# Performance work log

Measured on AMD Instinct MI355X. Metric: run time of the kernel, lower is better.

Reference implementation:

```python
import jax, jax.numpy as jnp
import numpy as np

EPS = 1e-12  # F.normalize eps


def setup_inputs() -> dict:
    key = jax.random.key(0)
    ks = jax.random.split(key, 12)
    N_NODES, N_EDGES, VOCAB, D = 100000, 1600000, 200000, 128
    return {
        "ent_embs": jax.random.normal(ks[0], (VOCAB, D), dtype=jnp.float32),
        "rel_embs": jax.random.normal(ks[1], (500, D), dtype=jnp.float32),
        "e_r_bias": jax.random.normal(ks[2], (N_NODES, D), dtype=jnp.float32),
        "out_norm": jax.random.uniform(ks[3], (N_NODES, 1), dtype=jnp.float32),
        "weight_neighbor": jax.random.normal(ks[4], (D, D), dtype=jnp.float32) * 0.05,
        "gru_w_ih": jax.random.normal(ks[5], (3 * D, 2 * D), dtype=jnp.float32) * 0.05,
        "gru_w_hh": jax.random.normal(ks[6], (3 * D, D), dtype=jnp.float32) * 0.05,
        "gru_b_ih": jnp.zeros((3 * D,), dtype=jnp.float32),
        "gru_b_hh": jnp.zeros((3 * D,), dtype=jnp.float32),
        "node_id": jax.random.randint(ks[7], (N_NODES,), 0, VOCAB, dtype=jnp.int64) if jax.config.jax_enable_x64 else jax.random.randint(ks[7], (N_NODES,), 0, VOCAB).astype(jnp.int32),
        "edge_src": jax.random.randint(ks[8], (N_EDGES,), 0, N_NODES).astype(jnp.int32),
        "edge_dst": jax.random.randint(ks[9], (N_EDGES,), 0, N_NODES).astype(jnp.int32),
        "g_idx": 0,
    }


def gru_cell(x, h, w_ih, w_hh, b_ih, b_hh):
    # torch.nn.GRUCell semantics; gates stacked as [r, z, n]
    gx = x @ w_ih.T + b_ih            # [N, 3D]
    gh = h @ w_hh.T + b_hh            # [N, 3D]
    xr, xz, xn = jnp.split(gx, 3, axis=1)
    hr, hz, hn = jnp.split(gh, 3, axis=1)
    r = jax.nn.sigmoid(xr + hr)
    z = jax.nn.sigmoid(xz + hz)
    n = jnp.tanh(xn + r * hn)
    return (1.0 - z) * n + z * h


def reference(ent_embs, rel_embs, e_r_bias, out_norm, weight_neighbor,
              gru_w_ih, gru_w_hh, gru_b_ih, gru_b_hh,
              node_id, edge_src, edge_dst, g_idx):
    n_nodes = e_r_bias.shape[0]
    # gather node embeddings, transform once per node (equivalent to per-edge mm)
    h = ent_embs[node_id]                       # [N, D]
    hW = h @ weight_neighbor                    # [N, D]
    msg = hW[edge_src]                          # [E, D] per-edge message
    agg = jax.ops.segment_sum(msg, edge_dst, num_segments=n_nodes)  # scatter-sum
    agg = agg * out_norm                        # apply_func: elementwise norm scale
    x = jnp.concatenate([agg, e_r_bias], axis=1)  # [N, 2D]
    # g_idx == 0 branch: hidden state is e_r_bias
    h0 = gru_cell(x, e_r_bias, gru_w_ih, gru_w_hh, gru_b_ih, gru_b_hh)
    h0 = jax.nn.relu(h0)
    # dropout is identity in eval mode
    norm = jnp.maximum(jnp.linalg.norm(h0, axis=1, keepdims=True), EPS)
    return h0 / norm
```

## Files before the change

### kernel.cpp

```cpp
#include <hip/hip_runtime.h>
#include <hip/hip_bf16.h>

#define D 128

typedef unsigned short u16;
typedef unsigned int   u32;
typedef unsigned long long u64;
typedef short bf16x8 __attribute__((ext_vector_type(8)));
typedef float f32x4  __attribute__((ext_vector_type(4)));

__device__ __forceinline__ float bf2f(u16 u) {
    union { u32 i; float f; } v; v.i = ((u32)u) << 16; return v.f;
}
__device__ __forceinline__ float bflo(u32 p) {
    union { u32 i; float f; } v; v.i = p << 16; return v.f;
}
__device__ __forceinline__ float bfhi(u32 p) {
    union { u32 i; float f; } v; v.i = p & 0xffff0000u; return v.f;
}
__device__ __forceinline__ u16 f2bf(float f) {
    union { float f; u32 i; } v; v.f = f;
    return (u16)((v.i + 0x7fffu + ((v.i >> 16) & 1u)) >> 16);
}
__device__ __forceinline__ float ldf(const void* p, long i, int isb) {
    return isb ? bf2f(((const u16*)p)[i]) : ((const float*)p)[i];
}

__device__ __forceinline__ float sigm(float x) { return 1.0f / (1.0f + __expf(-x)); }
__device__ __forceinline__ float tanh_fast(float x) {
    float a = fabsf(x);
    float t = __expf(-2.0f * a);
    float r = (1.0f - t) / (1.0f + t);
    return copysignf(r, x);
}

__global__ void DRlocal_net_79173427135059_kernel() {}

__global__ __launch_bounds__(64) void k_detect(const void* ent, const void* nid, int* flag) {
    int lane = threadIdx.x;
    float a = fabsf(bf2f(((const u16*)ent)[lane]));
    bool sane = (a >= 9.765625e-4f && a <= 64.0f);
    u64 m = __ballot(sane);
    u32 w = ((const u32*)nid)[lane];
    bool oddzero = ((lane & 1) == 0) || (w == 0u);
    u64 m2 = __ballot(oddzero);
    if (lane == 0) {
        flag[0] = (__popcll(m) >= 48) ? 1 : 0;
        flag[1] = (m2 == ~0ull) ? 1 : 0;
    }
}

__global__ __launch_bounds__(256) void k_prep(
    const void* __restrict__ w_ih, const void* __restrict__ w_hh,
    const void* __restrict__ b_ih, const void* __restrict__ b_hh,
    const void* __restrict__ W, const int* __restrict__ flag,
    u16* __restrict__ WTb, u16* __restrict__ Wihb, u16* __restrict__ Whhb,
    float* __restrict__ bif, float* __restrict__ bhf)
{
    int isb = flag[0];
    int t = blockIdx.x * 256 + threadIdx.x;
    if (t < 16384) {
        int k = t >> 7, j = t & 127;
        u16 v = isb ? ((const u16*)W)[t] : f2bf(((const float*)W)[t]);
        WTb[j * 128 + k] = v;
        return;
    }
    int u = t - 16384;
    if (u < 98304) { Wihb[u] = isb ? ((const u16*)w_ih)[u] : f2bf(((const float*)w_ih)[u]); return; }
    int v = u - 98304;
    if (v < 49152) { Whhb[v] = isb ? ((const u16*)w_hh)[v] : f2bf(((const float*)w_hh)[v]); return; }
    int b = v - 49152;
    if (b < 384) { bif[b] = ldf(b_ih, b, isb); return; }
    int c = b - 384;
    if (c < 384) { bhf[c] = ldf(b_hh, c, isb); return; }
}

__global__ __launch_bounds__(256) void k_zero(int* __restrict__ cnt, int n) {
    int t = blockIdx.x * 256 + threadIdx.x;
    if (t < n) cnt[t] = 0;
}

__global__ __launch_bounds__(256) void k_gmm_mfma(
    const void* __restrict__ ent, const void* __restrict__ node_id,
    const u16* __restrict__ WTb, u16* __restrict__ hW,
    const int* __restrict__ flag, int N)
{
    int isb = flag[0], i64 = flag[1];
    int tid = threadIdx.x;
    int wave = tid >> 6, lane = tid & 63;
    int qm = lane >> 4, qr = lane & 15;
    int row0 = blockIdx.x * 64 + wave * 16;

    int rowA = row0 + qr; if (rowA >= N) rowA = N - 1;
    long nid = i64 ? (long)((const long long*)node_id)[rowA]
                   : (long)((const int*)node_id)[rowA];

    bf16x8 a[4];
    if (isb) {
        const u16* ep = (const u16*)ent + nid * 128 + qm * 8;
        #pragma unroll
        for (int s = 0; s < 4; ++s) a[s] = *(const bf16x8*)(ep + s * 32);
    } else {
        const float* ep = (const float*)ent + nid * 128 + qm * 8;
        #pragma unroll
        for (int s = 0; s < 4; ++s) {
            float4 f0 = *(const float4*)(ep + s * 32);
            float4 f1 = *(const float4*)(ep + s * 32 + 4);
            bf16x8 t;
            t[0] = (short)f2bf(f0.x); t[1] = (short)f2bf(f0.y);
            t[2] = (short)f2bf(f0.z); t[3] = (short)f2bf(f0.w);
            t[4] = (short)f2bf(f1.x); t[5] = (short)f2bf(f1.y);
            t[6] = (short)f2bf(f1.z); t[7] = (short)f2bf(f1.w);
            a[s] = t;
        }
    }

    int r0 = row0 + qm * 4;
    #pragma unroll
    for (int f = 0; f < 8; ++f) {
        f32x4 acc = {0.f, 0.f, 0.f, 0.f};
        const u16* wp = WTb + (size_t)(f * 16 + qr) * 128 + qm * 8;
        #pragma unroll
        for (int s = 0; s < 4; ++s) {
            bf16x8 b = *(const bf16x8*)(wp + s * 32);
            acc = __builtin_amdgcn_mfma_f32_16x16x32_bf16(a[s], b, acc, 0, 0, 0);
        }
        int col = f * 16 + qr;
        #pragma unroll
        for (int r = 0; r < 4; ++r) {
            int row = r0 + r;
            if (row < N) hW[(size_t)row * 128 + col] = f2bf(acc[r]);
        }
    }
}

__global__ __launch_bounds__(256) void k_hist(
    const int* __restrict__ edst, int* __restrict__ cnt, int E)
{
    int e = blockIdx.x * 256 + threadIdx.x;
    if (e < E) atomicAdd(&cnt[edst[e]], 1);
}

__global__ __launch_bounds__(256) void k_scan1(
    const int* __restrict__ cnt, int* __restrict__ rowstart,
    int* __restrict__ part, int N)
{
    __shared__ int ssum[256];
    int b = blockIdx.x, t = threadIdx.x;
    int base = b * 1024 + t * 4;
    int v[4]; int s = 0;
    #pragma unroll
    for (int i = 0; i < 4; ++i) {
        int idx = base + i;
        v[i] = (idx < N) ? cnt[idx] : 0;
        s += v[i];
    }
    ssum[t] = s;
    __syncthreads();
    #pragma unroll
    for (int off = 1; off < 256; off <<= 1) {
        int x = (t >= off) ? ssum[t - off] : 0;
        __syncthreads();
        ssum[t] += x;
        __syncthreads();
    }
    int run = ssum[t] - s;
    #pragma unroll
    for (int i = 0; i < 4; ++i) {
        int idx = base + i;
        if (idx < N) rowstart[idx] = run;
        run += v[i];
    }
    if (t == 255) part[b] = ssum[255];
}

__global__ __launch_bounds__(128) void k_scan2(
    int* __restrict__ part, int* __restrict__ rowstart, int nb, int N)
{
    __shared__ int sh[128];
    int t = threadIdx.x;
    int run = 0;
    for (int base = 0; base < nb; base += 128) {
        int i = base + t;
        int v = (i < nb) ? part[i] : 0;
        sh[t] = v;
        __syncthreads();
        #pragma unroll
        for (int off = 1; off < 128; off <<= 1) {
            int x = (t >= off) ? sh[t - off] : 0;
            __syncthreads();
            sh[t] += x;
            __syncthreads();
        }
        int incl = sh[t];
        if (i < nb) part[i] = run + incl - v;
        int tot = sh[127];
        __syncthreads();
        run += tot;
    }
    if (t == 0) rowstart[N] = run;
}

__global__ __launch_bounds__(256) void k_scan3(
    int* __restrict__ rowstart, const int* __restrict__ part,
    int* __restrict__ cursor, int N)
{
    int t = blockIdx.x * 256 + threadIdx.x;
    if (t < N) {
        int r = rowstart[t] + part[t >> 10];
        rowstart[t] = r;
        cursor[t] = r;
    }
}

__global__ __launch_bounds__(256) void k_fill(
    const int* __restrict__ esrc, const int* __restrict__ edst,
    int* __restrict__ cursor, int* __restrict__ sorted_src, int E)
{
    int e = blockIdx.x * 256 + threadIdx.x;
    if (e < E) {
        int d = edst[e];
        int pos = atomicAdd(&cursor[d], 1);
        sorted_src[pos] = esrc[e];
    }
}

__global__ __launch_bounds__(256) void k_seg(
    const u16* __restrict__ hW, const int* __restrict__ rowstart,
    const int* __restrict__ sorted_src, const void* __restrict__ onorm,
    const void* __restrict__ bias, u16* __restrict__ X,
    const int* __restrict__ flag, int N)
{
    int isb = flag[0];
    int tid = threadIdx.x;
    int node = blockIdx.x * 4 + (tid >> 6);
    int lane = tid & 63;
    if (node >= N) return;
    int beg = rowstart[node], end = rowstart[node + 1];
    const u32* hw2 = (const u32*)hW;
    float a0 = 0.f, a1 = 0.f;
    int e = beg;
    for (; e + 8 <= end; e += 8) {
        int sI[8]; u32 vI[8];
        #pragma unroll
        for (int i = 0; i < 8; ++i) sI[i] = sorted_src[e + i];
        #pragma unroll
        for (int i = 0; i < 8; ++i) vI[i] = hw2[(size_t)sI[i] * 64 + lane];
        #pragma unroll
        for (int i = 0; i < 8; ++i) { a0 += bflo(vI[i]); a1 += bfhi(vI[i]); }
    }
    for (; e + 4 <= end; e += 4) {
        int s0 = sorted_src[e], s1 = sorted_src[e + 1];
        int s2 = sorted_src[e + 2], s3 = sorted_src[e + 3];
        u32 v0 = hw2[(size_t)s0 * 64 + lane];
        u32 v1 = hw2[(size_t)s1 * 64 + lane];
        u32 v2 = hw2[(size_t)s2 * 64 + lane];
        u32 v3 = hw2[(size_t)s3 * 64 + lane];
        a0 += bflo(v0) + bflo(v1) + bflo(v2) + bflo(v3);
        a1 += bfhi(v0) + bfhi(v1) + bfhi(v2) + bfhi(v3);
    }
    for (; e < end; ++e) {
        u32 v = hw2[(size_t)sorted_src[e] * 64 + lane];
        a0 += bflo(v); a1 += bfhi(v);
    }
    float on = ldf(onorm, node, isb);
    u32 p = ((u32)f2bf(a1 * on) << 16) | (u32)f2bf(a0 * on);
    ((u32*)X)[(size_t)node * 128 + lane] = p;
    u32 pb;
    if (isb) pb = ((const u32*)bias)[(size_t)node * 64 + lane];
    else {
        const float* bp = (const float*)bias + (size_t)node * 128 + lane * 2;
        pb = ((u32)f2bf(bp[1]) << 16) | (u32)f2bf(bp[0]);
    }
    ((u32*)X)[(size_t)node * 128 + 64 + lane] = pb;
}

__global__ __launch_bounds__(512, 2) void k_gru_mfma(
    const u16* __restrict__ X, const u16* __restrict__ Wih,
    const u16* __restrict__ Whh, const float* __restrict__ bif,
    const float* __restrict__ bhf, void* __restrict__ out,
    float* __restrict__ ssb,
    const int* __restrict__ flag, int N, int NpadX)
{
    __shared__ alignas(16) char smem[147456];
    int isb = flag[0];
    int tid = threadIdx.x;
    int wave = tid >> 6, lane = tid & 63;
    int qm = lane >> 4, qr = lane & 15;
    int g = blockIdx.x & 1;
    int chunk = blockIdx.x >> 1;
    int g64 = g * 64;

    for (int t = tid; t < 6144; t += 512) {
        int L = t * 16;
        int kb = L & 511;
        int c  = (L >> 9) & 63;
        int gi = L >> 15;
        int src = (gi * 128 + g64 + c) * 512 + kb;
        int dst = L ^ ((c & 7) << 4);
        *(bf16x8*)(smem + dst) = *(const bf16x8*)((const char*)Wih + src);
    }
    for (int t = tid; t < 3072; t += 512) {
        int L = t * 16;
        int kb = L & 255;
        int c  = (L >> 8) & 63;
        int gi = L >> 14;
        int src = (gi * 128 + g64 + c) * 256 + kb;
        int dst = 98304 + (L ^ ((c & 7) << 4));
        *(bf16x8*)(smem + dst) = *(const bf16x8*)((const char*)Whh + src);
    }
    __syncthreads();

    int rbase = chunk * 256 + wave * 32;

    bf16x8 aA[8], aB[8];
    {
        const u16* x0 = X + (size_t)(rbase + qr) * 256 + qm * 8;
        #pragma unroll
        for (int s = 0; s < 8; ++s) aA[s] = *(const bf16x8*)(x0 + s * 32);
        const u16* x1 = x0 + 16 * 256;
        #pragma unroll
        for (int s = 0; s < 8; ++s) aB[s] = *(const bf16x8*)(x1 + s * 32);
    }

    float ss[8] = {0.f, 0.f, 0.f, 0.f, 0.f, 0.f, 0.f, 0.f};

    #pragma unroll 1
    for (int sl = 0; sl < 4; ++sl) {
        int colIdx = sl * 16 + qr;
        int colg = g64 + colIdx;
        int sw = (qr & 7) << 4;
        int cbI = colIdx * 512 + qm * 16;
        int cbH = colIdx * 256 + qm * 16;

        f32x4 zz = {0.f, 0.f, 0.f, 0.f};
        f32x4 aR0 = zz, aR1 = zz, aZ0 = zz, aZ1 = zz;
        f32x4 aN0 = zz, aN1 = zz, aH0 = zz, aH1 = zz;

        {
            bf16x8 w[12];
            #pragma unroll
            for (int s = 0; s < 8; ++s)
                w[s] = *(const bf16x8*)(smem + ((cbI + s * 64) ^ sw));
            #pragma unroll
            for (int s = 0; s < 4; ++s)
                w[8 + s] = *(const bf16x8*)(smem + 98304 + ((cbH + s * 64) ^ sw));
            #pragma unroll
            for (int s = 0; s < 8; ++s) {
                aR0 = __builtin_amdgcn_mfma_f32_16x16x32_bf16(aA[s], w[s], aR0, 0, 0, 0);
                aR1 = __builtin_amdgcn_mfma_f32_16x16x32_bf16(aB[s], w[s], aR1, 0, 0, 0);
            }
            #pragma unroll
            for (int s = 0; s < 4; ++s) {
                aR0 = __builtin_amdgcn_mfma_f32_16x16x32_bf16(aA[4 + s], w[8 + s], aR0, 0, 0, 0);
                aR1 = __builtin_amdgcn_mfma_f32_16x16x32_bf16(aB[4 + s], w[8 + s], aR1, 0, 0, 0);
            }
        }
        {
            bf16x8 w[12];
            #pragma unroll
            for (int s = 0; s < 8; ++s)
                w[s] = *(const bf16x8*)(smem + 32768 + ((cbI + s * 64) ^ sw));
            #pragma unroll
            for (int s = 0; s < 4; ++s)
                w[8 + s] = *(const bf16x8*)(smem + 98304 + 16384 + ((cbH + s * 64) ^ sw));
            #pragma unroll
            for (int s = 0; s < 8; ++s) {
                aZ0 = __builtin_amdgcn_mfma_f32_16x16x32_bf16(aA[s], w[s], aZ0, 0, 0, 0);
                aZ1 = __builtin_amdgcn_mfma_f32_16x16x32_bf16(aB[s], w[s], aZ1, 0, 0, 0);
            }
            #pragma unroll
            for (int s = 0; s < 4; ++s) {
                aZ0 = __builtin_amdgcn_mfma_f32_16x16x32_bf16(aA[4 + s], w[8 + s], aZ0, 0, 0, 0);
                aZ1 = __builtin_amdgcn_mfma_f32_16x16x32_bf16(aB[4 + s], w[8 + s], aZ1, 0, 0, 0);
            }
        }
        {
            bf16x8 w[12];
            #pragma unroll
            for (int s = 0; s < 8; ++s)
                w[s] = *(const bf16x8*)(smem + 65536 + ((cbI + s * 64) ^ sw));
            #pragma unroll
            for (int s = 0; s < 4; ++s)
                w[8 + s] = *(const bf16x8*)(smem + 98304 + 32768 + ((cbH + s * 64) ^ sw));
            #pragma unroll
            for (int s = 0; s < 8; ++s) {
                aN0 = __builtin_amdgcn_mfma_f32_16x16x32_bf16(aA[s], w[s], aN0, 0, 0, 0);
                aN1 = __builtin_amdgcn_mfma_f32_16x16x32_bf16(aB[s], w[s], aN1, 0, 0, 0);
            }
            #pragma unroll
            for (int s = 0; s < 4; ++s) {
                aH0 = __builtin_amdgcn_mfma_f32_16x16x32_bf16(aA[4 + s], w[8 + s], aH0, 0, 0, 0);
                aH1 = __builtin_amdgcn_mfma_f32_16x16x32_bf16(aB[4 + s], w[8 + s], aH1, 0, 0, 0);
            }
        }

        float brz = bif[colg] + bhf[colg];
        float bzz = bif[128 + colg] + bhf[128 + colg];
        float bnx = bif[256 + colg];
        float bnh = bhf[256 + colg];

        #pragma unroll
        for (int ms = 0; ms < 2; ++ms) {
            #pragma unroll
            for (int r = 0; r < 4; ++r) {
                float vR = ms ? aR1[r] : aR0[r];
                float vZ = ms ? aZ1[r] : aZ0[r];
                float vN = ms ? aN1[r] : aN0[r];
                float vH = ms ? aH1[r] : aH0[r];
                int row = rbase + ms * 16 + qm * 4 + r;
                float rg = sigm(vR + brz);
                float z  = sigm(vZ + bzz);
                float ng = tanh_fast(vN + bnx + rg * (vH + bnh));
                float h  = bf2f(X[(size_t)row * 256 + 128 + colg]);
                float h0 = fmaxf((1.f - z) * ng + z * h, 0.f);
                if (row < N) {
                    if (isb) ((u16*)out)[(size_t)row * 128 + colg] = f2bf(h0);
                    else     ((float*)out)[(size_t)row * 128 + colg] = h0;
                }
                ss[ms * 4 + r] += h0 * h0;
            }
        }
    }

    #pragma unroll
    for (int i = 0; i < 8; ++i) {
        float s = ss[i];
        s += __shfl_xor(s, 1, 64);
        s += __shfl_xor(s, 2, 64);
        s += __shfl_xor(s, 4, 64);
        s += __shfl_xor(s, 8, 64);
        ss[i] = s;
    }
    if (qr == 0) {
        #pragma unroll
        for (int ms = 0; ms < 2; ++ms)
            #pragma unroll
            for (int r = 0; r < 4; ++r)
                ssb[(size_t)g * NpadX + rbase + ms * 16 + qm * 4 + r] = ss[ms * 4 + r];
    }
}

__global__ __launch_bounds__(256) void k_norm(
    void* __restrict__ out, const float* __restrict__ ssb,
    const int* __restrict__ flag, int N, int NpadX)
{
    int isb = flag[0];
    int tid = threadIdx.x;
    int wave = tid >> 6, lane = tid & 63;
    int row = blockIdx.x * 16 + wave * 4 + (lane >> 4);
    if (row >= N) return;
    int c8 = (lane & 15) * 8;
    float s = ssb[row] + ssb[(size_t)NpadX + row];
    float iv = 1.f / fmaxf(sqrtf(s), 1e-12f);
    if (isb) {
        u16* p = (u16*)out + (size_t)row * 128 + c8;
        bf16x8 v = *(const bf16x8*)p;
        bf16x8 o;
        #pragma unroll
        for (int j = 0; j < 8; ++j) o[j] = (short)f2bf(bf2f((u16)v[j]) * iv);
        *(bf16x8*)p = o;
    } else {
        float* p = (float*)out + (size_t)row * 128 + c8;
        float4 v0 = *(float4*)p, v1 = *(float4*)(p + 4);
        v0.x *= iv; v0.y *= iv; v0.z *= iv; v0.w *= iv;
        v1.x *= iv; v1.y *= iv; v1.z *= iv; v1.w *= iv;
        *(float4*)p = v0; *(float4*)(p + 4) = v1;
    }
}

extern "C" void kernel_launch(void* const* d_in, const int* in_sizes, int n_in,
                              void* d_out, int out_size, void* d_ws, size_t ws_size,
                              hipStream_t stream) {
    const void* ent     = d_in[0];
    const void* bias    = d_in[2];
    const void* onorm   = d_in[3];
    const void* W       = d_in[4];
    const void* w_ih    = d_in[5];
    const void* w_hh    = d_in[6];
    const void* b_ih    = d_in[7];
    const void* b_hh    = d_in[8];
    const void* node_id = d_in[9];
    const int*  esrc    = (const int*)d_in[10];
    const int*  edst    = (const int*)d_in[11];

    int N = in_sizes[2] / D;
    int E = in_sizes[10];
    int NpadX = ((N + 255) / 256) * 256;

    char* ws = (char*)d_ws;
    size_t o = 0;
    int*   flag = (int*)(ws + o);   o += 64;
    u16*   WTb  = (u16*)(ws + o);   o += 16384u * 2;
    u16*   Wihb = (u16*)(ws + o);   o += 98304u * 2;
    u16*   Whhb = (u16*)(ws + o);   o += 49152u * 2;
    float* bif  = (float*)(ws + o); o += 2048;
    float* bhf  = (float*)(ws + o); o += 2048;
    u16*   X    = (u16*)(ws + o);   o += (size_t)NpadX * 256 * 2;
    u16*   hW   = (u16*)(ws + o);   o += (size_t)N * D * 2;
    int*   cnt  = (int*)(ws + o);   o += (size_t)N * 4;
    int*   rowstart = (int*)(ws + o); o += ((size_t)N + 16) * 4;
    int*   part = (int*)(ws + o);   o += 4096;
    int*   sorted_src = (int*)(ws + o); o += (size_t)E * 4;
    int*   cursor = cnt;
    float* ssb = (float*)sorted_src;

    int nb = (N + 1023) / 1024;
    int nchunk = NpadX / 256;

    k_detect<<<1, 64, 0, stream>>>(ent, node_id, flag);
    k_prep<<<643, 256, 0, stream>>>(w_ih, w_hh, b_ih, b_hh, W, flag,
                                    WTb, Wihb, Whhb, bif, bhf);
    k_zero<<<(N + 255) / 256, 256, 0, stream>>>(cnt, N);
    k_gmm_mfma<<<(N + 63) / 64, 256, 0, stream>>>(ent, node_id, WTb, hW, flag, N);
    k_hist<<<(E + 255) / 256, 256, 0, stream>>>(edst, cnt, E);
    k_scan1<<<nb, 256, 0, stream>>>(cnt, rowstart, part, N);
    k_scan2<<<1, 128, 0, stream>>>(part, rowstart, nb, N);
    k_scan3<<<(N + 255) / 256, 256, 0, stream>>>(rowstart, part, cursor, N);
    k_fill<<<(E + 255) / 256, 256, 0, stream>>>(esrc, edst, cursor, sorted_src, E);
    k_seg<<<(N + 3) / 4, 256, 0, stream>>>(hW, rowstart, sorted_src, onorm, bias, X, flag, N);
    k_gru_mfma<<<nchunk * 2, 512, 0, stream>>>(X, Wihb, Whhb, bif, bhf, d_out, ssb, flag, N, NpadX);
    k_norm<<<(N + 15) / 16, 256, 0, stream>>>(d_out, ssb, flag, N, NpadX);
}
```

Measured before the change: 622.4 us.

## Replace global-atomic CSR build with two-level bucketed counting sort

Builds the destination-sorted edge list by bucketing edges into groups of up to 512 node ranges using shared-memory histograms, then sorting within each bucket in LDS. This replaces per-edge global atomics on 100k counters plus a three-kernel scan and a random scatter fill. The aim is fewer global atomics and kernel launches, and more local scatter writes. The cost is an extra pass that writes packed 64-bit edge pairs into a buffer that reuses the X workspace, and only 391 blocks in the per-bucket sort.

```diff
diff --git a/kernel.cpp b/kernel.cpp
--- a/kernel.cpp
+++ b/kernel.cpp
@@ -36,8 +36,10 @@
 
 __global__ void DRlocal_net_79173427135059_kernel() {}
 
-__global__ __launch_bounds__(64) void k_detect(const void* ent, const void* nid, int* flag) {
+__global__ __launch_bounds__(64) void k_detect(const void* ent, const void* nid,
+                                               int* flag, int* bhist) {
     int lane = threadIdx.x;
+    for (int i = lane; i < 512; i += 64) bhist[i] = 0;
     float a = fabsf(bf2f(((const u16*)ent)[lane]));
     bool sane = (a >= 9.765625e-4f && a <= 64.0f);
     u64 m = __ballot(sane);
@@ -75,11 +77,6 @@
     if (c < 384) { bhf[c] = ldf(b_hh, c, isb); return; }
 }
 
-__global__ __launch_bounds__(256) void k_zero(int* __restrict__ cnt, int n) {
-    int t = blockIdx.x * 256 + threadIdx.x;
-    if (t < n) cnt[t] = 0;
-}
-
 __global__ __launch_bounds__(256) void k_gmm_mfma(
     const void* __restrict__ ent, const void* __restrict__ node_id,
     const u16* __restrict__ WTb, u16* __restrict__ hW,
@@ -134,94 +131,132 @@
     }
 }
 
-__global__ __launch_bounds__(256) void k_hist(
-    const int* __restrict__ edst, int* __restrict__ cnt, int E)
-{
-    int e = blockIdx.x * 256 + threadIdx.x;
-    if (e < E) atomicAdd(&cnt[edst[e]], 1);
-}
-
-__global__ __launch_bounds__(256) void k_scan1(
-    const int* __restrict__ cnt, int* __restrict__ rowstart,
-    int* __restrict__ part, int N)
-{
-    __shared__ int ssum[256];
+
+__global__ __launch_bounds__(256) void k_bhist(
+    const int* __restrict__ edst, int* __restrict__ bhist,
+    int E, int NB, int bshift)
+{
+    __shared__ int lcnt[512];
+    int t = threadIdx.x;
+    int e0 = blockIdx.x * 8192;
+    for (int i = t; i < NB; i += 256) lcnt[i] = 0;
+    __syncthreads();
+    for (int i = t; i < 8192; i += 256) {
+        int e = e0 + i;
+        if (e < E) atomicAdd(&lcnt[edst[e] >> bshift], 1);
+    }
+    __syncthreads();
+    for (int i = t; i < NB; i += 256) {
+        int c = lcnt[i];
+        if (c) atomicAdd(&bhist[i], c);
+    }
+}
+
+__global__ __launch_bounds__(512) void k_bscan(
+    const int* __restrict__ bhist, int* __restrict__ bstart,
+    int* __restrict__ bcur, int* __restrict__ rowstart,
+    int NB, int N, int E)
+{
+    __shared__ int sh[512];
+    int t = threadIdx.x;
+    int v = (t < NB) ? bhist[t] : 0;
+    sh[t] = v;
+    __syncthreads();
+    #pragma unroll
+    for (int off = 1; off < 512; off <<= 1) {
+        int x = (t >= off) ? sh[t - off] : 0;
+        __syncthreads();
+        sh[t] += x;
+        __syncthreads();
+    }
+    int excl = sh[t] - v;
+    if (t < NB) { bstart[t] = excl; bcur[t] = excl; }
+    if (t == 0) { bstart[NB] = E; rowstart[N] = E; }
+}
+
+__global__ __launch_bounds__(256) void k_afill(
+    const int* __restrict__ esrc, const int* __restrict__ edst,
+    int* __restrict__ bcur, u64* __restrict__ ebuf,
+    int E, int NB, int bshift)
+{
+    __shared__ int lcnt[512];
+    int t = threadIdx.x;
+    int e0 = blockIdx.x * 8192;
+    for (int i = t; i < NB; i += 256) lcnt[i] = 0;
+    __syncthreads();
+    for (int i = t; i < 8192; i += 256) {
+        int e = e0 + i;
+        if (e < E) atomicAdd(&lcnt[edst[e] >> bshift], 1);
+    }
+    __syncthreads();
+    for (int b = t; b < NB; b += 256) {
+        int c = lcnt[b];
+        lcnt[b] = c ? atomicAdd(&bcur[b], c) : 0;
+    }
+    __syncthreads();
+    for (int i = t; i < 8192; i += 256) {
+        int e = e0 + i;
+        if (e < E) {
+            int d = edst[e];
+            int pos = atomicAdd(&lcnt[d >> bshift], 1);
+            ebuf[pos] = ((u64)(u32)esrc[e] << 32) | (u32)d;
+        }
+    }
+}
+
+__global__ __launch_bounds__(256) void k_bfill(
+    const u64* __restrict__ ebuf, const int* __restrict__ bstart,
+    int* __restrict__ rowstart, int* __restrict__ sorted_src,
+    int N, int bshift)
+{
+    __shared__ int lcnt[1024];
+    __shared__ int lscan[256];
     int b = blockIdx.x, t = threadIdx.x;
-    int base = b * 1024 + t * 4;
-    int v[4]; int s = 0;
+    int nodes = 1 << bshift;
+    int per = nodes >> 8;
+    int base = b << bshift;
+    int beg = bstart[b], end = bstart[b + 1];
+
+    for (int i = t; i < nodes; i += 256) lcnt[i] = 0;
+    __syncthreads();
+    for (int i = beg + t; i < end; i += 256) {
+        int d = (int)(u32)ebuf[i];
+        atomicAdd(&lcnt[d - base], 1);
+    }
+    __syncthreads();
+
+    int myv[4]; int mysum = 0;
     #pragma unroll
-    for (int i = 0; i < 4; ++i) {
-        int idx = base + i;
-        v[i] = (idx < N) ? cnt[idx] : 0;
-        s += v[i];
-    }
-    ssum[t] = s;
+    for (int j = 0; j < 4; ++j) {
+        myv[j] = (j < per) ? lcnt[t * per + j] : 0;
+        mysum += myv[j];
+    }
+    lscan[t] = mysum;
     __syncthreads();
     #pragma unroll
     for (int off = 1; off < 256; off <<= 1) {
-        int x = (t >= off) ? ssum[t - off] : 0;
+        int x = (t >= off) ? lscan[t - off] : 0;
         __syncthreads();
-        ssum[t] += x;
+        lscan[t] += x;
         __syncthreads();
     }
-    int run = ssum[t] - s;
+    int run = beg + lscan[t] - mysum;
     #pragma unroll
-    for (int i = 0; i < 4; ++i) {
-        int idx = base + i;
-        if (idx < N) rowstart[idx] = run;
-        run += v[i];
-    }
-    if (t == 255) part[b] = ssum[255];
-}
-
-__global__ __launch_bounds__(128) void k_scan2(
-    int* __restrict__ part, int* __restrict__ rowstart, int nb, int N)
-{
-    __shared__ int sh[128];
-    int t = threadIdx.x;
-    int run = 0;
-    for (int base = 0; base < nb; base += 128) {
-        int i = base + t;
-        int v = (i < nb) ? part[i] : 0;
-        sh[t] = v;
-        __syncthreads();
-        #pragma unroll
-        for (int off = 1; off < 128; off <<= 1) {
-            int x = (t >= off) ? sh[t - off] : 0;
-            __syncthreads();
-            sh[t] += x;
-            __syncthreads();
-        }
-        int incl = sh[t];
-        if (i < nb) part[i] = run + incl - v;
-        int tot = sh[127];
-        __syncthreads();
-        run += tot;
-    }
-    if (t == 0) rowstart[N] = run;
-}
-
-__global__ __launch_bounds__(256) void k_scan3(
-    int* __restrict__ rowstart, const int* __restrict__ part,
-    int* __restrict__ cursor, int N)
-{
-    int t = blockIdx.x * 256 + threadIdx.x;
-    if (t < N) {
-        int r = rowstart[t] + part[t >> 10];
-        rowstart[t] = r;
-        cursor[t] = r;
-    }
-}
-
-__global__ __launch_bounds__(256) void k_fill(
-    const int* __restrict__ esrc, const int* __restrict__ edst,
-    int* __restrict__ cursor, int* __restrict__ sorted_src, int E)
-{
-    int e = blockIdx.x * 256 + threadIdx.x;
-    if (e < E) {
-        int d = edst[e];
-        int pos = atomicAdd(&cursor[d], 1);
-        sorted_src[pos] = esrc[e];
+    for (int j = 0; j < 4; ++j) {
+        if (j < per) {
+            int idx = t * per + j;
+            int node = base + idx;
+            if (node < N) rowstart[node] = run;
+            lcnt[idx] = run;
+            run += myv[j];
+        }
+    }
+    __syncthreads();
+    for (int i = beg + t; i < end; i += 256) {
+        u64 p = ebuf[i];
+        int d = (int)(u32)p;
+        int pos = atomicAdd(&lcnt[d - base], 1);
+        sorted_src[pos] = (int)(p >> 32);
     }
 }
 
@@ -488,6 +523,10 @@
     int E = in_sizes[10];
     int NpadX = ((N + 255) / 256) * 256;
 
+    int bshift = 8;
+    while ((((N - 1) >> bshift) + 1) > 512) bshift++;
+    int NB = ((N - 1) >> bshift) + 1;
+
     char* ws = (char*)d_ws;
     size_t o = 0;
     int*   flag = (int*)(ws + o);   o += 64;
@@ -498,26 +537,25 @@
     float* bhf  = (float*)(ws + o); o += 2048;
     u16*   X    = (u16*)(ws + o);   o += (size_t)NpadX * 256 * 2;
     u16*   hW   = (u16*)(ws + o);   o += (size_t)N * D * 2;
-    int*   cnt  = (int*)(ws + o);   o += (size_t)N * 4;
+    int*   bhist = (int*)(ws + o);  o += 512 * 4;
+    int*   bstart = (int*)(ws + o); o += 514 * 4;
+    int*   bcur  = (int*)(ws + o);  o += 512 * 4;
     int*   rowstart = (int*)(ws + o); o += ((size_t)N + 16) * 4;
-    int*   part = (int*)(ws + o);   o += 4096;
     int*   sorted_src = (int*)(ws + o); o += (size_t)E * 4;
-    int*   cursor = cnt;
+    u64*   ebuf = (u64*)X;
     float* ssb = (float*)sorted_src;
 
-    int nb = (N + 1023) / 1024;
     int nchunk = NpadX / 256;
-
-    k_detect<<<1, 64, 0, stream>>>(ent, node_id, flag);
+    int nA = (E + 8191) / 8192;
+
+    k_detect<<<1, 64, 0, stream>>>(ent, node_id, flag, bhist);
     k_prep<<<643, 256, 0, stream>>>(w_ih, w_hh, b_ih, b_hh, W, flag,
                                     WTb, Wihb, Whhb, bif, bhf);
-    k_zero<<<(N + 255) / 256, 256, 0, stream>>>(cnt, N);
     k_gmm_mfma<<<(N + 63) / 64, 256, 0, stream>>>(ent, node_id, WTb, hW, flag, N);
-    k_hist<<<(E + 255) / 256, 256, 0, stream>>>(edst, cnt, E);
-    k_scan1<<<nb, 256, 0, stream>>>(cnt, rowstart, part, N);
-    k_scan2<<<1, 128, 0, stream>>>(part, rowstart, nb, N);
-    k_scan3<<<(N + 255) / 256, 256, 0, stream>>>(rowstart, part, cursor, N);
-    k_fill<<<(E + 255) / 256, 256, 0, stream>>>(esrc, edst, cursor, sorted_src, E);
+    k_bhist<<<nA, 256, 0, stream>>>(edst, bhist, E, NB, bshift);
+    k_bscan<<<1, 512, 0, stream>>>(bhist, bstart, bcur, rowstart, NB, N, E);
+    k_afill<<<nA, 256, 0, stream>>>(esrc, edst, bcur, ebuf, E, NB, bshift);
+    k_bfill<<<NB, 256, 0, stream>>>(ebuf, bstart, rowstart, sorted_src, N, bshift);
     k_seg<<<(N + 3) / 4, 256, 0, stream>>>(hW, rowstart, sorted_src, onorm, bias, X, flag, N);
     k_gru_mfma<<<nchunk * 2, 512, 0, stream>>>(X, Wihb, Whhb, bif, bhf, d_out, ssb, flag, N, NpadX);
     k_norm<<<(N + 15) / 16, 256, 0, stream>>>(d_out, ssb, flag, N, NpadX);
```

Result: faster. 508.1 us (-18.4%).
